# Kernel optimization log

Measured on AMD Instinct MI355X. Metric: run time of the kernel, lower is better.

Reference implementation:

```python
import jax, jax.numpy as jnp
import numpy as np

B = 32768
IN_F = 256
OUT_F = 256


def setup_inputs() -> dict:
    key = jax.random.key(0)
    k1, k2 = jax.random.split(key)
    x = jax.random.normal(k1, (B, IN_F, 4), dtype=jnp.float32)
    std = 1.0 / np.sqrt(4 * IN_F)
    weight = jax.random.normal(k2, (OUT_F, IN_F, 4), dtype=jnp.float32) * std
    weight = weight.at[..., 0].add(0.5)  # quaternion Xavier: bias real part
    bias = jnp.zeros((OUT_F, 4), dtype=jnp.float32)
    return {"x": x, "weight": weight, "bias": bias}


def _quat_linear(x, weight, bias):
    # x: (..., in, 4) with components (w, x, y, z); weight: (out, in, 4)
    # Hamilton product q1=W, q2=x, summed over in -> 16 structured matmuls.
    xw, xx, xy, xz = x[..., 0], x[..., 1], x[..., 2], x[..., 3]
    ww, wx, wy, wz = weight[..., 0], weight[..., 1], weight[..., 2], weight[..., 3]

    def mm(w, v):  # (out, in) x (..., in) -> (..., out)
        return jnp.einsum('oi,...i->...o', w, v)

    yw = mm(ww, xw) - mm(wx, xx) - mm(wy, xy) - mm(wz, xz)
    yx = mm(ww, xx) + mm(wx, xw) + mm(wy, xz) - mm(wz, xy)
    yy = mm(ww, xy) - mm(wx, xz) + mm(wy, xw) + mm(wz, xx)
    yz = mm(ww, xz) + mm(wx, xy) - mm(wy, xx) + mm(wz, xw)

    y = jnp.stack([yw, yx, yy, yz], axis=-1)  # (..., out, 4)
    return y + bias


def reference(x, weight, bias):
    return _quat_linear(x, weight, bias)
```

## Files before the change

kernel.cpp:

```cpp
#include <hip/hip_runtime.h>


typedef __bf16 bf16x8_t __attribute__((ext_vector_type(8)));
typedef short short8    __attribute__((ext_vector_type(8)));
typedef float f32x4     __attribute__((ext_vector_type(4)));
typedef float f32x8     __attribute__((ext_vector_type(8)));

typedef const unsigned int __attribute__((address_space(1)))* gas_uint_ptr;
typedef unsigned int __attribute__((address_space(3)))*       las_uint_ptr;

__global__ __launch_bounds__(256) void build_weff(const float* __restrict__ w,
                                                  unsigned short* __restrict__ wq) {
    int idx = blockIdx.x * 256 + threadIdx.x;
    int n = idx >> 10, k = idx & 1023;
    int o = n >> 2, r = n & 3, i = k >> 2, c = k & 3;
    int s = r ^ c;
    float v = w[o * 1024 + i * 4 + s];
    if ((0x284E >> (r * 4 + c)) & 1) v = -v;
    union { __bf16 b; unsigned short u; } cv;
    cv.b = (__bf16)v;
    wq[idx] = cv.u;
}

__global__ __launch_bounds__(256) void conv_x(const float* __restrict__ x,
                                              unsigned short* __restrict__ xb) {
    const long long c = (long long)blockIdx.x * 256 + threadIdx.x;
    const float* gp = x + c * 8;
    f32x4 lo = *(const f32x4*)gp;
    f32x4 hi = *(const f32x4*)(gp + 4);
    f32x8 f8 = __builtin_shufflevector(lo, hi, 0, 1, 2, 3, 4, 5, 6, 7);
    bf16x8_t bv = __builtin_convertvector(f8, bf16x8_t);
    union { bf16x8_t b; short8 s; } cv;
    cv.b = bv;
    *(short8*)(xb + c * 8) = cv.s;
}

__global__ __launch_bounds__(512, 2) void qlin_gemm_8ph(
        const unsigned short* __restrict__ Xb,
        const unsigned short* __restrict__ Wq,
        const float* __restrict__ bias,
        float* __restrict__ out) {
    __shared__ __align__(16) unsigned short As[2][2][128 * 64];
    __shared__ __align__(16) unsigned short Bs[2][2][128 * 64];

    const int t    = threadIdx.x;
    const int w    = t >> 6;
    const int l    = t & 63;
    const int lo16 = l & 15;
    const int hi2  = l >> 4;

    const int bid     = blockIdx.x;
    const int xcd     = bid & 7;
    const int logical = xcd * 64 + (bid >> 3);
    const int m0      = (logical >> 2) * 256;
    const int n0      = (logical & 3) * 256;

    const int wm  = (w >> 2) * 128;
    const int wn  = (w & 3) * 64;
    const int hA  = wm >> 7;
    const int hB  = wn >> 7;
    const int rbB = wn & 64;

    f32x4 acc[8][4] = {};
    short8 af[2][2];
    short8 bf[4][2];

    const int sw    = lo16 & 7;
    const int slot0 = hi2 ^ sw;
    const int slot1 = (4 + hi2) ^ sw;

#define STAGE_A(KT, H) do {                                                     \
        const int kk_ = ((KT) & 15) * 64;                                       \
        _Pragma("unroll")                                                       \
        for (int jj = 0; jj < 2; ++jj) {                                        \
            const int idx_ = jj * 512 + t;                                      \
            const int row_ = idx_ >> 3;                                         \
            const int g_   = (idx_ & 7) ^ (row_ & 7);                           \
            const unsigned short* ga_ =                                         \
                Xb + (long long)(m0 + (H) * 128 + row_) * 1024 + kk_ + g_ * 8;  \
            __builtin_amdgcn_global_load_lds((gas_uint_ptr)ga_,                 \
                (las_uint_ptr)(&As[(KT) & 1][(H)][idx_ * 8]), 16, 0, 0);        \
        }                                                                       \
    } while (0)

#define STAGE_B(KT, H) do {                                                     \
        const int kk_ = ((KT) & 15) * 64;                                       \
        _Pragma("unroll")                                                       \
        for (int jj = 0; jj < 2; ++jj) {                                        \
            const int idx_ = jj * 512 + t;                                      \
            const int row_ = idx_ >> 3;                                         \
            const int g_   = (idx_ & 7) ^ (row_ & 7);                           \
            const unsigned short* gb_ =                                         \
                Wq + (n0 + (H) * 128 + row_) * 1024 + kk_ + g_ * 8;             \
            __builtin_amdgcn_global_load_lds((gas_uint_ptr)gb_,                 \
                (las_uint_ptr)(&Bs[(KT) & 1][(H)][idx_ * 8]), 16, 0, 0);        \
        }                                                                       \
    } while (0)

#define READ_BF(PAR) do {                                                       \
        _Pragma("unroll")                                                       \
        for (int nt = 0; nt < 4; ++nt) {                                        \
            const int rl_ = rbB + nt * 16 + lo16;                               \
            bf[nt][0] = *(const short8*)(&Bs[(PAR)][hB][rl_ * 64 + slot0 * 8]); \
            bf[nt][1] = *(const short8*)(&Bs[(PAR)][hB][rl_ * 64 + slot1 * 8]); \
        }                                                                       \
    } while (0)

#define READ_AF(PAR, MTB) do {                                                  \
        _Pragma("unroll")                                                       \
        for (int mi = 0; mi < 2; ++mi) {                                        \
            const int rl_ = ((MTB) + mi) * 16 + lo16;                           \
            af[mi][0] = *(const short8*)(&As[(PAR)][hA][rl_ * 64 + slot0 * 8]); \
            af[mi][1] = *(const short8*)(&As[(PAR)][hA][rl_ * 64 + slot1 * 8]); \
        }                                                                       \
    } while (0)

#define MFMA_Q(MTB) do {                                                        \
        _Pragma("unroll")                                                       \
        for (int mi = 0; mi < 2; ++mi)                                          \
            _Pragma("unroll")                                                   \
            for (int nt = 0; nt < 4; ++nt) {                                    \
                acc[(MTB) + mi][nt] = __builtin_amdgcn_mfma_f32_16x16x32_bf16(  \
                    af[mi][0], bf[nt][0], acc[(MTB) + mi][nt], 0, 0, 0);        \
                acc[(MTB) + mi][nt] = __builtin_amdgcn_mfma_f32_16x16x32_bf16(  \
                    af[mi][1], bf[nt][1], acc[(MTB) + mi][nt], 0, 0, 0);        \
            }                                                                   \
    } while (0)

#define PHASE(PAR, MTB, RDB, ENDW, STAGE_STMT) do {                             \
        if (RDB) READ_BF(PAR);                                                  \
        READ_AF(PAR, MTB);                                                      \
        STAGE_STMT;                                                             \
        asm volatile("s_barrier" ::: "memory");                                 \
        asm volatile("s_waitcnt lgkmcnt(0)" ::: "memory");                      \
        __builtin_amdgcn_s_setprio(1);                                          \
        MFMA_Q(MTB);                                                            \
        __builtin_amdgcn_s_setprio(0);                                          \
        if (ENDW) asm volatile("s_waitcnt vmcnt(4)" ::: "memory");              \
        asm volatile("s_barrier" ::: "memory");                                 \
    } while (0)

    STAGE_B(0, 0); STAGE_B(0, 1);
    STAGE_A(0, 0); STAGE_A(0, 1);
    STAGE_B(1, 0); STAGE_B(1, 1);
    asm volatile("s_waitcnt vmcnt(4)" ::: "memory");
    asm volatile("s_barrier" ::: "memory");

    for (int i = 0; i < 8; ++i) {
        const int kt1 = 2 * i + 1;
        PHASE(0, 0, true,  false, STAGE_A(kt1, 0));
        PHASE(0, 2, false, false, STAGE_A(kt1, 1));
        PHASE(0, 4, false, false, STAGE_B(kt1 + 1, 0));
        PHASE(0, 6, false, true,  STAGE_B(kt1 + 1, 1));
        PHASE(1, 0, true,  false, STAGE_A(kt1 + 1, 0));
        PHASE(1, 2, false, false, STAGE_A(kt1 + 1, 1));
        PHASE(1, 4, false, false, STAGE_B(kt1 + 2, 0));
        PHASE(1, 6, false, true,  STAGE_B(kt1 + 2, 1));
    }

#undef STAGE_A
#undef STAGE_B
#undef READ_BF
#undef READ_AF
#undef MFMA_Q
#undef PHASE

#pragma unroll
    for (int nt = 0; nt < 4; ++nt) {
        const int n  = n0 + wn + nt * 16 + lo16;
        const float bv = bias[n];
#pragma unroll
        for (int mt = 0; mt < 8; ++mt) {
            const int mb = m0 + wm + mt * 16 + hi2 * 4;
#pragma unroll
            for (int r = 0; r < 4; ++r)
                out[(long long)(mb + r) * 1024 + n] = acc[mt][nt][r] + bv;
        }
    }
}

__global__ __launch_bounds__(256) void qlin_gemm_fused(const float* __restrict__ X,
                                                       const unsigned short* __restrict__ Wq,
                                                       const float* __restrict__ bias,
                                                       float* __restrict__ out) {
    __shared__ __align__(16) unsigned short As[128 * 64];
    __shared__ __align__(16) unsigned short Bs[128 * 64];

    const int t    = threadIdx.x;
    const int w    = t >> 6;
    const int l    = t & 63;
    const int lo16 = l & 15;
    const int hi2  = l >> 4;
    const int bid  = blockIdx.x;
    const int xcd  = bid & 7;
    const int s    = bid >> 3;
    const int m0   = (xcd * 32 + (s >> 3)) * 128;
    const int n0   = (s & 7) * 128;
    const int wm   = (w & 1) * 64;
    const int wn   = (w >> 1) * 64;

    f32x4 acc[4][4] = {};

    for (int kt = 0; kt < 16; ++kt) {
        const int k0 = kt * 64;
        __syncthreads();
#pragma unroll
        for (int jj = 0; jj < 4; ++jj) {
            const int p    = jj * 256 + t;
            const int row  = p >> 3;
            const int g    = (p & 7) ^ (row & 7);
            const unsigned short* gp = Wq + (n0 + row) * 1024 + k0 + g * 8;
            __builtin_amdgcn_global_load_lds((gas_uint_ptr)gp,
                                             (las_uint_ptr)(Bs + p * 8), 16, 0, 0);
        }
#pragma unroll
        for (int jj = 0; jj < 4; ++jj) {
            const int c    = jj * 256 + t;
            const int row  = c >> 3;
            const int g    = c & 7;
            const float* gp = X + (long long)(m0 + row) * 1024 + k0 + g * 8;
            f32x4 lo = *(const f32x4*)gp;
            f32x4 hi = *(const f32x4*)(gp + 4);
            f32x8 f8 = __builtin_shufflevector(lo, hi, 0, 1, 2, 3, 4, 5, 6, 7);
            bf16x8_t bv = __builtin_convertvector(f8, bf16x8_t);
            union { bf16x8_t b; short8 s; } cv;
            cv.b = bv;
            const int p = row * 8 + (g ^ (row & 7));
            *(short8*)(As + p * 8) = cv.s;
        }
        __syncthreads();
#pragma unroll
        for (int ks = 0; ks < 2; ++ks) {
            const int g = ks * 4 + hi2;
            short8 af[4], bf[4];
#pragma unroll
            for (int mt = 0; mt < 4; ++mt) {
                const int r = wm + mt * 16 + lo16;
                af[mt] = *(const short8*)(As + (r * 8 + (g ^ (r & 7))) * 8);
            }
#pragma unroll
            for (int nt = 0; nt < 4; ++nt) {
                const int r = wn + nt * 16 + lo16;
                bf[nt] = *(const short8*)(Bs + (r * 8 + (g ^ (r & 7))) * 8);
            }
#pragma unroll
            for (int mt = 0; mt < 4; ++mt)
#pragma unroll
                for (int nt = 0; nt < 4; ++nt)
                    acc[mt][nt] = __builtin_amdgcn_mfma_f32_16x16x32_bf16(
                        af[mt], bf[nt], acc[mt][nt], 0, 0, 0);
        }
    }

#pragma unroll
    for (int nt = 0; nt < 4; ++nt) {
        const int n  = n0 + wn + nt * 16 + lo16;
        const float bv = bias[n];
#pragma unroll
        for (int mt = 0; mt < 4; ++mt) {
            const int mb = m0 + wm + mt * 16 + hi2 * 4;
#pragma unroll
            for (int r = 0; r < 4; ++r)
                out[(long long)(mb + r) * 1024 + n] = acc[mt][nt][r] + bv;
        }
    }
}

extern "C" void kernel_launch(void* const* d_in, const int* in_sizes, int n_in,
                              void* d_out, int out_size, void* d_ws, size_t ws_size,
                              hipStream_t stream) {
    const float* x  = (const float*)d_in[0];
    const float* wt = (const float*)d_in[1];
    const float* bs = (const float*)d_in[2];
    float* out = (float*)d_out;

    unsigned short* wq = (unsigned short*)d_ws;
    const size_t WQ_BYTES = 1024ull * 1024 * 2;
    const size_t XB_BYTES = 32768ull * 1024 * 2;

    build_weff<<<4096, 256, 0, stream>>>(wt, wq);

    if (ws_size >= WQ_BYTES + XB_BYTES) {
        unsigned short* xb = (unsigned short*)((char*)d_ws + WQ_BYTES);
        conv_x<<<16384, 256, 0, stream>>>(x, xb);
        qlin_gemm_8ph<<<512, 512, 0, stream>>>(xb, wq, bs, out);
    } else {
        qlin_gemm_fused<<<2048, 256, 0, stream>>>(x, wq, bs, out);
    }

    (void)in_sizes; (void)n_in; (void)out_size;
}
```

Measured before the change: 305.5 us.

## Merge prep kernels and restructure GEMM main loop into two barrier phases

Fuses the weight-expansion and x-to-bf16 conversion kernels into one launch, which removes a kernel launch and its tail gap. The GEMM main loop changes from eight barrier-separated phases per two k-tiles to two phases per k-tile. All A fragments for a k-tile are preloaded into registers so more MFMAs issue between barriers. This adds register pressure from the larger A fragment array and changes the order of staging relative to reads, which risks LDS hazards and spills at 2 waves per SIMD.

Measured after the change: 307.3 us. Within noise of the previous version (+0.6%).

```diff
diff --git a/kernel.cpp b/kernel.cpp
--- a/kernel.cpp
+++ b/kernel.cpp
@@ -9,33 +9,45 @@
 typedef const unsigned int __attribute__((address_space(1)))* gas_uint_ptr;
 typedef unsigned int __attribute__((address_space(3)))*       las_uint_ptr;
 
-__global__ __launch_bounds__(256) void build_weff(const float* __restrict__ w,
-                                                  unsigned short* __restrict__ wq) {
-    int idx = blockIdx.x * 256 + threadIdx.x;
-    int n = idx >> 10, k = idx & 1023;
-    int o = n >> 2, r = n & 3, i = k >> 2, c = k & 3;
-    int s = r ^ c;
+__device__ __forceinline__ void weff_body(const float* __restrict__ w,
+                                          unsigned short* __restrict__ wq,
+                                          int idx) {
+    const int n = idx >> 10, k = idx & 1023;
+    const int o = n >> 2, r = n & 3, i = k >> 2, cc = k & 3;
+    const int s = r ^ cc;
     float v = w[o * 1024 + i * 4 + s];
-    if ((0x284E >> (r * 4 + c)) & 1) v = -v;
+    if ((0x284E >> (r * 4 + cc)) & 1) v = -v;
     union { __bf16 b; unsigned short u; } cv;
     cv.b = (__bf16)v;
     wq[idx] = cv.u;
 }
 
-__global__ __launch_bounds__(256) void conv_x(const float* __restrict__ x,
-                                              unsigned short* __restrict__ xb) {
-    const long long c = (long long)blockIdx.x * 256 + threadIdx.x;
-    const float* gp = x + c * 8;
-    f32x4 lo = *(const f32x4*)gp;
-    f32x4 hi = *(const f32x4*)(gp + 4);
-    f32x8 f8 = __builtin_shufflevector(lo, hi, 0, 1, 2, 3, 4, 5, 6, 7);
-    bf16x8_t bv = __builtin_convertvector(f8, bf16x8_t);
-    union { bf16x8_t b; short8 s; } cv;
-    cv.b = bv;
-    *(short8*)(xb + c * 8) = cv.s;
-}
-
-__global__ __launch_bounds__(512, 2) void qlin_gemm_8ph(
+__global__ __launch_bounds__(256) void prep(const float* __restrict__ x,
+                                            unsigned short* __restrict__ xb,
+                                            const float* __restrict__ w,
+                                            unsigned short* __restrict__ wq) {
+    const int b = blockIdx.x;
+    if (b < 16384) {
+        const long long c = (long long)b * 256 + threadIdx.x;
+        const float* gp = x + c * 8;
+        f32x4 lo = *(const f32x4*)gp;
+        f32x4 hi = *(const f32x4*)(gp + 4);
+        f32x8 f8 = __builtin_shufflevector(lo, hi, 0, 1, 2, 3, 4, 5, 6, 7);
+        bf16x8_t bv = __builtin_convertvector(f8, bf16x8_t);
+        union { bf16x8_t b; short8 s; } cv;
+        cv.b = bv;
+        *(short8*)(xb + c * 8) = cv.s;
+    } else {
+        weff_body(w, wq, (b - 16384) * 256 + threadIdx.x);
+    }
+}
+
+__global__ __launch_bounds__(256) void build_weff(const float* __restrict__ w,
+                                                  unsigned short* __restrict__ wq) {
+    weff_body(w, wq, blockIdx.x * 256 + threadIdx.x);
+}
+
+__global__ __launch_bounds__(512, 2) void qlin_gemm_quad(
         const unsigned short* __restrict__ Xb,
         const unsigned short* __restrict__ Wq,
         const float* __restrict__ bias,
@@ -62,7 +74,7 @@
     const int rbB = wn & 64;
 
     f32x4 acc[8][4] = {};
-    short8 af[2][2];
+    short8 afq[4][2][2];
     short8 bf[4][2];
 
     const int sw    = lo16 & 7;
@@ -106,38 +118,27 @@
         }                                                                       \
     } while (0)
 
-#define READ_AF(PAR, MTB) do {                                                  \
+#define READ_AFQ(PAR, Q) do {                                                   \
         _Pragma("unroll")                                                       \
         for (int mi = 0; mi < 2; ++mi) {                                        \
-            const int rl_ = ((MTB) + mi) * 16 + lo16;                           \
-            af[mi][0] = *(const short8*)(&As[(PAR)][hA][rl_ * 64 + slot0 * 8]); \
-            af[mi][1] = *(const short8*)(&As[(PAR)][hA][rl_ * 64 + slot1 * 8]); \
+            const int rl_ = ((Q) * 2 + mi) * 16 + lo16;                         \
+            afq[(Q)][mi][0] =                                                   \
+                *(const short8*)(&As[(PAR)][hA][rl_ * 64 + slot0 * 8]);         \
+            afq[(Q)][mi][1] =                                                   \
+                *(const short8*)(&As[(PAR)][hA][rl_ * 64 + slot1 * 8]);         \
         }                                                                       \
     } while (0)
 
-#define MFMA_Q(MTB) do {                                                        \
+#define MFMA_Q(Q) do {                                                          \
         _Pragma("unroll")                                                       \
         for (int mi = 0; mi < 2; ++mi)                                          \
             _Pragma("unroll")                                                   \
             for (int nt = 0; nt < 4; ++nt) {                                    \
-                acc[(MTB) + mi][nt] = __builtin_amdgcn_mfma_f32_16x16x32_bf16(  \
-                    af[mi][0], bf[nt][0], acc[(MTB) + mi][nt], 0, 0, 0);        \
-                acc[(MTB) + mi][nt] = __builtin_amdgcn_mfma_f32_16x16x32_bf16(  \
-                    af[mi][1], bf[nt][1], acc[(MTB) + mi][nt], 0, 0, 0);        \
+                acc[(Q) * 2 + mi][nt] = __builtin_amdgcn_mfma_f32_16x16x32_bf16(\
+                    afq[(Q)][mi][0], bf[nt][0], acc[(Q) * 2 + mi][nt], 0, 0, 0);\
+                acc[(Q) * 2 + mi][nt] = __builtin_amdgcn_mfma_f32_16x16x32_bf16(\
+                    afq[(Q)][mi][1], bf[nt][1], acc[(Q) * 2 + mi][nt], 0, 0, 0);\
             }                                                                   \
-    } while (0)
-
-#define PHASE(PAR, MTB, RDB, ENDW, STAGE_STMT) do {                             \
-        if (RDB) READ_BF(PAR);                                                  \
-        READ_AF(PAR, MTB);                                                      \
-        STAGE_STMT;                                                             \
-        asm volatile("s_barrier" ::: "memory");                                 \
-        asm volatile("s_waitcnt lgkmcnt(0)" ::: "memory");                      \
-        __builtin_amdgcn_s_setprio(1);                                          \
-        MFMA_Q(MTB);                                                            \
-        __builtin_amdgcn_s_setprio(0);                                          \
-        if (ENDW) asm volatile("s_waitcnt vmcnt(4)" ::: "memory");              \
-        asm volatile("s_barrier" ::: "memory");                                 \
     } while (0)
 
     STAGE_B(0, 0); STAGE_B(0, 1);
@@ -146,24 +147,42 @@
     asm volatile("s_waitcnt vmcnt(4)" ::: "memory");
     asm volatile("s_barrier" ::: "memory");
 
-    for (int i = 0; i < 8; ++i) {
-        const int kt1 = 2 * i + 1;
-        PHASE(0, 0, true,  false, STAGE_A(kt1, 0));
-        PHASE(0, 2, false, false, STAGE_A(kt1, 1));
-        PHASE(0, 4, false, false, STAGE_B(kt1 + 1, 0));
-        PHASE(0, 6, false, true,  STAGE_B(kt1 + 1, 1));
-        PHASE(1, 0, true,  false, STAGE_A(kt1 + 1, 0));
-        PHASE(1, 2, false, false, STAGE_A(kt1 + 1, 1));
-        PHASE(1, 4, false, false, STAGE_B(kt1 + 2, 0));
-        PHASE(1, 6, false, true,  STAGE_B(kt1 + 2, 1));
-    }
+    for (int kt = 0; kt < 16; ++kt) {
+        const int par = kt & 1;
+
+        READ_BF(par);
+        READ_AFQ(par, 0);
+        READ_AFQ(par, 1);
+        STAGE_A(kt + 1, 0);
+        STAGE_A(kt + 1, 1);
+
+        __builtin_amdgcn_s_setprio(1);
+        MFMA_Q(0);
+        __builtin_amdgcn_s_setprio(0);
+        __builtin_amdgcn_sched_barrier(0);
+        asm volatile("s_barrier" ::: "memory");
+
+        STAGE_B(kt + 2, 0);
+        STAGE_B(kt + 2, 1);
+        READ_AFQ(par, 2);
+        READ_AFQ(par, 3);
+
+        __builtin_amdgcn_s_setprio(1);
+        MFMA_Q(1);
+        MFMA_Q(2);
+        MFMA_Q(3);
+        __builtin_amdgcn_s_setprio(0);
+        __builtin_amdgcn_sched_barrier(0);
+        asm volatile("s_waitcnt vmcnt(4)" ::: "memory");
+        asm volatile("s_barrier" ::: "memory");
+    }
+    asm volatile("s_waitcnt vmcnt(0)" ::: "memory");
 
 #undef STAGE_A
 #undef STAGE_B
 #undef READ_BF
-#undef READ_AF
+#undef READ_AFQ
 #undef MFMA_Q
-#undef PHASE
 
 #pragma unroll
     for (int nt = 0; nt < 4; ++nt) {
@@ -232,7 +251,7 @@
 #pragma unroll
         for (int ks = 0; ks < 2; ++ks) {
             const int g = ks * 4 + hi2;
-            short8 af[4], bf[4];
+            short8 af[4], bfr[4];
 #pragma unroll
             for (int mt = 0; mt < 4; ++mt) {
                 const int r = wm + mt * 16 + lo16;
@@ -241,14 +260,14 @@
 #pragma unroll
             for (int nt = 0; nt < 4; ++nt) {
                 const int r = wn + nt * 16 + lo16;
-                bf[nt] = *(const short8*)(Bs + (r * 8 + (g ^ (r & 7))) * 8);
+                bfr[nt] = *(const short8*)(Bs + (r * 8 + (g ^ (r & 7))) * 8);
             }
 #pragma unroll
             for (int mt = 0; mt < 4; ++mt)
 #pragma unroll
                 for (int nt = 0; nt < 4; ++nt)
                     acc[mt][nt] = __builtin_amdgcn_mfma_f32_16x16x32_bf16(
-                        af[mt], bf[nt], acc[mt][nt], 0, 0, 0);
+                        af[mt], bfr[nt], acc[mt][nt], 0, 0, 0);
         }
     }
 
@@ -278,13 +297,12 @@
     const size_t WQ_BYTES = 1024ull * 1024 * 2;
     const size_t XB_BYTES = 32768ull * 1024 * 2;
 
-    build_weff<<<4096, 256, 0, stream>>>(wt, wq);
-
     if (ws_size >= WQ_BYTES + XB_BYTES) {
         unsigned short* xb = (unsigned short*)((char*)d_ws + WQ_BYTES);
-        conv_x<<<16384, 256, 0, stream>>>(x, xb);
-        qlin_gemm_8ph<<<512, 512, 0, stream>>>(xb, wq, bs, out);
+        prep<<<20480, 256, 0, stream>>>(x, xb, wt, wq);
+        qlin_gemm_quad<<<512, 512, 0, stream>>>(xb, wq, bs, out);
     } else {
+        build_weff<<<4096, 256, 0, stream>>>(wt, wq);
         qlin_gemm_fused<<<2048, 256, 0, stream>>>(x, wq, bs, out);
     }
 
```

## Fuse fp32-to-bf16 conversion of X into pipelined GEMM A-tile staging

Applied to the files above, without the earlier changes.

Removes the separate conversion kernel and bf16 workspace copy of X; the GEMM now loads fp32 X tiles into registers, converts to bf16, and writes swizzled rows into LDS within the existing 8-phase pipeline. This eliminates a full read/write pass over the activations and a launch. It trades the async global-to-LDS path for register-staged loads, raising register pressure and doubling the bytes read for A inside the GEMM.

New measurement: 313.4 us. +2.6%, slower.

```diff
diff --git a/kernel.cpp b/kernel.cpp
--- a/kernel.cpp
+++ b/kernel.cpp
@@ -11,32 +11,19 @@
 
 __global__ __launch_bounds__(256) void build_weff(const float* __restrict__ w,
                                                   unsigned short* __restrict__ wq) {
-    int idx = blockIdx.x * 256 + threadIdx.x;
-    int n = idx >> 10, k = idx & 1023;
-    int o = n >> 2, r = n & 3, i = k >> 2, c = k & 3;
-    int s = r ^ c;
+    const int idx = blockIdx.x * 256 + threadIdx.x;
+    const int n = idx >> 10, k = idx & 1023;
+    const int o = n >> 2, r = n & 3, i = k >> 2, cc = k & 3;
+    const int s = r ^ cc;
     float v = w[o * 1024 + i * 4 + s];
-    if ((0x284E >> (r * 4 + c)) & 1) v = -v;
+    if ((0x284E >> (r * 4 + cc)) & 1) v = -v;
     union { __bf16 b; unsigned short u; } cv;
     cv.b = (__bf16)v;
     wq[idx] = cv.u;
 }
 
-__global__ __launch_bounds__(256) void conv_x(const float* __restrict__ x,
-                                              unsigned short* __restrict__ xb) {
-    const long long c = (long long)blockIdx.x * 256 + threadIdx.x;
-    const float* gp = x + c * 8;
-    f32x4 lo = *(const f32x4*)gp;
-    f32x4 hi = *(const f32x4*)(gp + 4);
-    f32x8 f8 = __builtin_shufflevector(lo, hi, 0, 1, 2, 3, 4, 5, 6, 7);
-    bf16x8_t bv = __builtin_convertvector(f8, bf16x8_t);
-    union { bf16x8_t b; short8 s; } cv;
-    cv.b = bv;
-    *(short8*)(xb + c * 8) = cv.s;
-}
-
-__global__ __launch_bounds__(512, 2) void qlin_gemm_8ph(
-        const unsigned short* __restrict__ Xb,
+__global__ __launch_bounds__(512, 2) void qlin_gemm_f32a(
+        const float* __restrict__ Xf,
         const unsigned short* __restrict__ Wq,
         const float* __restrict__ bias,
         float* __restrict__ out) {
@@ -49,6 +36,10 @@
     const int lo16 = l & 15;
     const int hi2  = l >> 4;
 
+    const int rsub = t >> 3;
+    const int g8   = t & 7;
+    const int sgA  = g8 ^ (rsub & 7);
+
     const int bid     = blockIdx.x;
     const int xcd     = bid & 7;
     const int logical = xcd * 64 + (bid >> 3);
@@ -64,23 +55,29 @@
     f32x4 acc[8][4] = {};
     short8 af[2][2];
     short8 bf[4][2];
+    f32x4 rA0[4], rA1[4];
 
     const int sw    = lo16 & 7;
     const int slot0 = hi2 ^ sw;
     const int slot1 = (4 + hi2) ^ sw;
 
-#define STAGE_A(KT, H) do {                                                     \
-        const int kk_ = ((KT) & 15) * 64;                                       \
-        _Pragma("unroll")                                                       \
-        for (int jj = 0; jj < 2; ++jj) {                                        \
-            const int idx_ = jj * 512 + t;                                      \
-            const int row_ = idx_ >> 3;                                         \
-            const int g_   = (idx_ & 7) ^ (row_ & 7);                           \
-            const unsigned short* ga_ =                                         \
-                Xb + (long long)(m0 + (H) * 128 + row_) * 1024 + kk_ + g_ * 8;  \
-            __builtin_amdgcn_global_load_lds((gas_uint_ptr)ga_,                 \
-                (las_uint_ptr)(&As[(KT) & 1][(H)][idx_ * 8]), 16, 0, 0);        \
-        }                                                                       \
+#define LOAD_A(KT, H, R) do {                                                   \
+        const float* ga_ = Xf + ((long long)(m0 + (H) * 128 + rsub) << 10)      \
+                              + (((KT) & 15) << 6) + (g8 << 3);                 \
+        R[0] = *(const f32x4*)ga_;                                              \
+        R[1] = *(const f32x4*)(ga_ + 4);                                        \
+        R[2] = *(const f32x4*)(ga_ + 65536);                      \
+        R[3] = *(const f32x4*)(ga_ + 65540);                                    \
+    } while (0)
+
+#define WRITE_A(KT, H, R) do {                                                  \
+        f32x8 lo_ = __builtin_shufflevector(R[0], R[1], 0, 1, 2, 3, 4, 5, 6, 7);\
+        f32x8 hi_ = __builtin_shufflevector(R[2], R[3], 0, 1, 2, 3, 4, 5, 6, 7);\
+        union { bf16x8_t b; short8 s; } c0_, c1_;                               \
+        c0_.b = __builtin_convertvector(lo_, bf16x8_t);                         \
+        c1_.b = __builtin_convertvector(hi_, bf16x8_t);                         \
+        *(short8*)(&As[(KT) & 1][(H)][(rsub * 8 + sgA) * 8]) = c0_.s;           \
+        *(short8*)(&As[(KT) & 1][(H)][((64 + rsub) * 8 + sgA) * 8]) = c1_.s;    \
     } while (0)
 
 #define STAGE_B(KT, H) do {                                                     \
@@ -115,7 +112,7 @@
         }                                                                       \
     } while (0)
 
-#define MFMA_Q(MTB) do {                                                        \
+#define MFMA_H(MTB) do {                                                        \
         _Pragma("unroll")                                                       \
         for (int mi = 0; mi < 2; ++mi)                                          \
             _Pragma("unroll")                                                   \
@@ -127,43 +124,81 @@
             }                                                                   \
     } while (0)
 
-#define PHASE(PAR, MTB, RDB, ENDW, STAGE_STMT) do {                             \
-        if (RDB) READ_BF(PAR);                                                  \
-        READ_AF(PAR, MTB);                                                      \
-        STAGE_STMT;                                                             \
-        asm volatile("s_barrier" ::: "memory");                                 \
-        asm volatile("s_waitcnt lgkmcnt(0)" ::: "memory");                      \
+#define BAR()   asm volatile("s_barrier" ::: "memory")
+#define LGKM0() asm volatile("s_waitcnt lgkmcnt(0)" ::: "memory")
+
+#define PHASE_TAIL(MTB) do {                                                    \
+        BAR(); LGKM0();                                                         \
         __builtin_amdgcn_s_setprio(1);                                          \
-        MFMA_Q(MTB);                                                            \
+        MFMA_H(MTB);                                                            \
         __builtin_amdgcn_s_setprio(0);                                          \
-        if (ENDW) asm volatile("s_waitcnt vmcnt(4)" ::: "memory");              \
-        asm volatile("s_barrier" ::: "memory");                                 \
+        BAR();                                                                  \
     } while (0)
 
     STAGE_B(0, 0); STAGE_B(0, 1);
-    STAGE_A(0, 0); STAGE_A(0, 1);
+    LOAD_A(0, 0, rA0);
+    LOAD_A(0, 1, rA1);
     STAGE_B(1, 0); STAGE_B(1, 1);
     asm volatile("s_waitcnt vmcnt(4)" ::: "memory");
-    asm volatile("s_barrier" ::: "memory");
+    WRITE_A(0, 0, rA0);
+    WRITE_A(0, 1, rA1);
+    LGKM0();
+    BAR();
 
     for (int i = 0; i < 8; ++i) {
         const int kt1 = 2 * i + 1;
-        PHASE(0, 0, true,  false, STAGE_A(kt1, 0));
-        PHASE(0, 2, false, false, STAGE_A(kt1, 1));
-        PHASE(0, 4, false, false, STAGE_B(kt1 + 1, 0));
-        PHASE(0, 6, false, true,  STAGE_B(kt1 + 1, 1));
-        PHASE(1, 0, true,  false, STAGE_A(kt1 + 1, 0));
-        PHASE(1, 2, false, false, STAGE_A(kt1 + 1, 1));
-        PHASE(1, 4, false, false, STAGE_B(kt1 + 2, 0));
-        PHASE(1, 6, false, true,  STAGE_B(kt1 + 2, 1));
+
+        READ_BF(0); READ_AF(0, 0);
+        LOAD_A(kt1, 0, rA0);
+        PHASE_TAIL(0);
+
+        READ_AF(0, 2);
+        LOAD_A(kt1, 1, rA1);
+        PHASE_TAIL(2);
+
+        READ_AF(0, 4);
+        STAGE_B(kt1 + 1, 0);
+        asm volatile("s_waitcnt vmcnt(6)" ::: "memory");
+        WRITE_A(kt1, 0, rA0);
+        PHASE_TAIL(4);
+
+        READ_AF(0, 6);
+        STAGE_B(kt1 + 1, 1);
+        asm volatile("s_waitcnt vmcnt(4)" ::: "memory");
+        WRITE_A(kt1, 1, rA1);
+        PHASE_TAIL(6);
+
+        READ_BF(1); READ_AF(1, 0);
+        LOAD_A(kt1 + 1, 0, rA0);
+        PHASE_TAIL(0);
+
+        READ_AF(1, 2);
+        LOAD_A(kt1 + 1, 1, rA1);
+        PHASE_TAIL(2);
+
+        READ_AF(1, 4);
+        STAGE_B(kt1 + 2, 0);
+        asm volatile("s_waitcnt vmcnt(6)" ::: "memory");
+        WRITE_A(kt1 + 1, 0, rA0);
+        PHASE_TAIL(4);
+
+        READ_AF(1, 6);
+        STAGE_B(kt1 + 2, 1);
+        asm volatile("s_waitcnt vmcnt(4)" ::: "memory");
+        WRITE_A(kt1 + 1, 1, rA1);
+        PHASE_TAIL(6);
     }
-
-#undef STAGE_A
+    asm volatile("s_waitcnt vmcnt(0)" ::: "memory");
+
+#undef LOAD_A
+#undef WRITE_A
 #undef STAGE_B
 #undef READ_BF
 #undef READ_AF
-#undef MFMA_Q
-#undef PHASE
+#undef MFMA_H
+#undef BAR
+#undef LGKM0
+#undef PHASE_TAIL
 
 #pragma unroll
     for (int nt = 0; nt < 4; ++nt) {
@@ -179,93 +214,6 @@
     }
 }
 
-__global__ __launch_bounds__(256) void qlin_gemm_fused(const float* __restrict__ X,
-                                                       const unsigned short* __restrict__ Wq,
-                                                       const float* __restrict__ bias,
-                                                       float* __restrict__ out) {
-    __shared__ __align__(16) unsigned short As[128 * 64];
-    __shared__ __align__(16) unsigned short Bs[128 * 64];
-
-    const int t    = threadIdx.x;
-    const int w    = t >> 6;
-    const int l    = t & 63;
-    const int lo16 = l & 15;
-    const int hi2  = l >> 4;
-    const int bid  = blockIdx.x;
-    const int xcd  = bid & 7;
-    const int s    = bid >> 3;
-    const int m0   = (xcd * 32 + (s >> 3)) * 128;
-    const int n0   = (s & 7) * 128;
-    const int wm   = (w & 1) * 64;
-    const int wn   = (w >> 1) * 64;
-
-    f32x4 acc[4][4] = {};
-
-    for (int kt = 0; kt < 16; ++kt) {
-        const int k0 = kt * 64;
-        __syncthreads();
-#pragma unroll
-        for (int jj = 0; jj < 4; ++jj) {
-            const int p    = jj * 256 + t;
-            const int row  = p >> 3;
-            const int g    = (p & 7) ^ (row & 7);
-            const unsigned short* gp = Wq + (n0 + row) * 1024 + k0 + g * 8;
-            __builtin_amdgcn_global_load_lds((gas_uint_ptr)gp,
-                                             (las_uint_ptr)(Bs + p * 8), 16, 0, 0);
-        }
-#pragma unroll
-        for (int jj = 0; jj < 4; ++jj) {
-            const int c    = jj * 256 + t;
-            const int row  = c >> 3;
-            const int g    = c & 7;
-            const float* gp = X + (long long)(m0 + row) * 1024 + k0 + g * 8;
-            f32x4 lo = *(const f32x4*)gp;
-            f32x4 hi = *(const f32x4*)(gp + 4);
-            f32x8 f8 = __builtin_shufflevector(lo, hi, 0, 1, 2, 3, 4, 5, 6, 7);
-            bf16x8_t bv = __builtin_convertvector(f8, bf16x8_t);
-            union { bf16x8_t b; short8 s; } cv;
-            cv.b = bv;
-            const int p = row * 8 + (g ^ (row & 7));
-            *(short8*)(As + p * 8) = cv.s;
-        }
-        __syncthreads();
-#pragma unroll
-        for (int ks = 0; ks < 2; ++ks) {
-            const int g = ks * 4 + hi2;
-            short8 af[4], bf[4];
-#pragma unroll
-            for (int mt = 0; mt < 4; ++mt) {
-                const int r = wm + mt * 16 + lo16;
-                af[mt] = *(const short8*)(As + (r * 8 + (g ^ (r & 7))) * 8);
-            }
-#pragma unroll
-            for (int nt = 0; nt < 4; ++nt) {
-                const int r = wn + nt * 16 + lo16;
-                bf[nt] = *(const short8*)(Bs + (r * 8 + (g ^ (r & 7))) * 8);
-            }
-#pragma unroll
-            for (int mt = 0; mt < 4; ++mt)
-#pragma unroll
-                for (int nt = 0; nt < 4; ++nt)
-                    acc[mt][nt] = __builtin_amdgcn_mfma_f32_16x16x32_bf16(
-                        af[mt], bf[nt], acc[mt][nt], 0, 0, 0);
-        }
-    }
-
-#pragma unroll
-    for (int nt = 0; nt < 4; ++nt) {
-        const int n  = n0 + wn + nt * 16 + lo16;
-        const float bv = bias[n];
-#pragma unroll
-        for (int mt = 0; mt < 4; ++mt) {
-            const int mb = m0 + wm + mt * 16 + hi2 * 4;
-#pragma unroll
-            for (int r = 0; r < 4; ++r)
-                out[(long long)(mb + r) * 1024 + n] = acc[mt][nt][r] + bv;
-        }
-    }
-}
-
 extern "C" void kernel_launch(void* const* d_in, const int* in_sizes, int n_in,
                               void* d_out, int out_size, void* d_ws, size_t ws_size,
                               hipStream_t stream) {
@@ -275,18 +223,9 @@
     float* out = (float*)d_out;
 
     unsigned short* wq = (unsigned short*)d_ws;
-    const size_t WQ_BYTES = 1024ull * 1024 * 2;
-    const size_t XB_BYTES = 32768ull * 1024 * 2;
 
     build_weff<<<4096, 256, 0, stream>>>(wt, wq);
-
-    if (ws_size >= WQ_BYTES + XB_BYTES) {
-        unsigned short* xb = (unsigned short*)((char*)d_ws + WQ_BYTES);
-        conv_x<<<16384, 256, 0, stream>>>(x, xb);
-        qlin_gemm_8ph<<<512, 512, 0, stream>>>(xb, wq, bs, out);
-    } else {
-        qlin_gemm_fused<<<2048, 256, 0, stream>>>(x, wq, bs, out);
-    }
-
-    (void)in_sizes; (void)n_in; (void)out_size;
+    qlin_gemm_f32a<<<512, 512, 0, stream>>>(x, wq, bs, out);
+
+    (void)in_sizes; (void)n_in; (void)out_size; (void)ws_size;
 }
```
